# Kernel optimization log

Hardware: AMD Instinct MI355X
Metric: run time of the kernel (lower is better)

Reference implementation:

```python
import jax, jax.numpy as jnp
import numpy as np

C = 256

def setup_inputs() -> dict:
    key = jax.random.key(0)
    ks = jax.random.split(key, 7)
    s = 1.0 / np.sqrt(C)
    x = jax.random.normal(ks[0], (4, C, 64, 64), dtype=jnp.float32)
    Wq = jax.random.uniform(ks[1], (C, C), jnp.float32, -s, s)
    bq = jax.random.uniform(ks[2], (C,), jnp.float32, -s, s)
    Wk = jax.random.uniform(ks[3], (C, C), jnp.float32, -s, s)
    bk = jax.random.uniform(ks[4], (C,), jnp.float32, -s, s)
    Wv = jax.random.uniform(ks[5], (C, C), jnp.float32, -s, s)
    bv = jax.random.uniform(ks[6], (C,), jnp.float32, -s, s)
    return {"x": x, "Wq": Wq, "bq": bq, "Wk": Wk, "bk": bk, "Wv": Wv, "bv": bv}

def reference(x, Wq, bq, Wk, bk, Wv, bv):
    B, Cc, H, W = x.shape
    N = H * W
    xf = x.reshape(B, Cc, N)                      # (B, C, N)
    # 1x1 conv == channel linear: out[b,o,n] = sum_c W[o,c] x[b,c,n] + b[o]
    q = jnp.einsum('oc,bcn->bno', Wq, xf) + bq    # (B, N, C)  proj_query^T
    k = jnp.einsum('oc,bcn->bon', Wk, xf) + bk[None, :, None]  # (B, C, N)
    v = jnp.einsum('oc,bcn->bon', Wv, xf) + bv[None, :, None]  # (B, C, N)
    energy = jnp.einsum('bnc,bcm->bnm', q, k)     # (B, N, N)
    attention = jax.nn.softmax(energy, axis=-1)
    # out = V @ attention^T : out[b,c,n] = sum_m v[b,c,m] * attention[b,n,m]
    out = jnp.einsum('bcm,bnm->bcn', v, attention)
    return out.reshape(B, Cc, H, W)
```

## Files before the change

kernel.cpp:

```cpp
#include <hip/hip_runtime.h>
#include <math.h>

#define BB 4
#define CC 256
#define NN 4096

using half8 = __attribute__((ext_vector_type(8))) _Float16;
using f32x4 = __attribute__((ext_vector_type(4))) float;

__device__ __forceinline__ unsigned short f2h(float f) {
  _Float16 h = (_Float16)f;
  return __builtin_bit_cast(unsigned short, h);
}

#define ASYNC16(g, l)                                                        \
  __builtin_amdgcn_global_load_lds(                                          \
      (const __attribute__((address_space(1))) unsigned int*)(g),            \
      (__attribute__((address_space(3))) unsigned int*)(l), 16, 0, 0)

__device__ __forceinline__ int kt_off(int r, int chunk) {
  return r * 256 + (((chunk & 24) | ((chunk ^ r) & 7)) << 3);
}
__device__ __forceinline__ int vt_off(int r, int chunk) {
  return r * 64 + (((chunk ^ r) & 7) << 3);
}

__global__ __launch_bounds__(256) void k_transpose(const float* __restrict__ x,
                                                   unsigned short* __restrict__ Xt) {
  __shared__ float tile[64][65];
  int b = blockIdx.z, c0 = blockIdx.y * 64, n0 = blockIdx.x * 64;
  int t = threadIdx.x;
  const float* xp = x + ((size_t)b * CC + c0) * NN + n0;
#pragma unroll
  for (int p = 0; p < 4; ++p) {
    int c = p * 16 + (t >> 4);
    int j = (t & 15) * 4;
    float4 v = *(const float4*)(xp + (size_t)c * NN + j);
    tile[c][j] = v.x; tile[c][j + 1] = v.y; tile[c][j + 2] = v.z; tile[c][j + 3] = v.w;
  }
  __syncthreads();
  unsigned short* xtp = Xt + ((size_t)b * NN + n0) * CC + c0;
#pragma unroll
  for (int p = 0; p < 2; ++p) {
    int n = p * 32 + (t >> 3);
    int cb = (t & 7) * 8;
    union { unsigned short u[8]; uint4 v; } tmp;
#pragma unroll
    for (int i = 0; i < 8; ++i) tmp.u[i] = f2h(tile[cb + i][n]);
    *(uint4*)(xtp + (size_t)n * CC + cb) = tmp.v;
  }
}

__global__ __launch_bounds__(256, 1) void k_proj(const unsigned short* __restrict__ Xt,
    const float* __restrict__ Wq, const float* __restrict__ bq,
    const float* __restrict__ Wk, const float* __restrict__ bk,
    const float* __restrict__ Wv, const float* __restrict__ bv,
    unsigned short* __restrict__ Q, unsigned short* __restrict__ K,
    unsigned short* __restrict__ V) {
  __shared__ union {
    struct { unsigned short xa[128][72]; unsigned short wb[256][72]; } s;
    unsigned short qo[128][264];
    unsigned short vo[256][136];
  } u;
  int proj = blockIdx.z;
  const float* W    = proj == 0 ? Wq : (proj == 1 ? Wk : Wv);
  const float* bias = proj == 0 ? bq : (proj == 1 ? bk : bv);
  int b = blockIdx.y, n0 = blockIdx.x * 128;
  int t = threadIdx.x, w = t >> 6, lane = t & 63, l15 = lane & 15, quad = lane >> 4;

  f32x4 z = {0.f, 0.f, 0.f, 0.f};
  f32x4 acc[2][16];
#pragma unroll
  for (int i = 0; i < 2; ++i)
#pragma unroll
    for (int j = 0; j < 16; ++j) acc[i][j] = z;

  for (int ks = 0; ks < 4; ++ks) {
    __syncthreads();
#pragma unroll
    for (int p = 0; p < 4; ++p) {
      int r = p * 32 + (t >> 3);
      *(uint4*)&u.s.xa[r][(t & 7) * 8] =
        *(const uint4*)(Xt + ((size_t)b * NN + n0 + r) * CC + ks * 64 + (t & 7) * 8);
    }
#pragma unroll
    for (int p = 0; p < 16; ++p) {
      int r = p * 16 + (t >> 4);
      float4 wv = *(const float4*)(W + (size_t)r * CC + ks * 64 + (t & 15) * 4);
      ushort4 pk;
      pk.x = f2h(wv.x); pk.y = f2h(wv.y); pk.z = f2h(wv.z); pk.w = f2h(wv.w);
      *(ushort4*)&u.s.wb[r][(t & 15) * 4] = pk;
    }
    __syncthreads();
#pragma unroll
    for (int kc = 0; kc < 2; ++kc) {
      half8 af[2];
#pragma unroll
      for (int nt = 0; nt < 2; ++nt)
        af[nt] = *(const half8*)&u.s.xa[w * 32 + nt * 16 + l15][kc * 32 + quad * 8];
#pragma unroll
      for (int ct = 0; ct < 16; ++ct) {
        half8 bf = *(const half8*)&u.s.wb[ct * 16 + l15][kc * 32 + quad * 8];
        acc[0][ct] = __builtin_amdgcn_mfma_f32_16x16x32_f16(af[0], bf, acc[0][ct], 0, 0, 0);
        acc[1][ct] = __builtin_amdgcn_mfma_f32_16x16x32_f16(af[1], bf, acc[1][ct], 0, 0, 0);
      }
    }
  }
#pragma unroll
  for (int ct = 0; ct < 16; ++ct) {
    float bv_ = bias[ct * 16 + l15];
#pragma unroll
    for (int nt = 0; nt < 2; ++nt)
#pragma unroll
      for (int r = 0; r < 4; ++r) acc[nt][ct][r] += bv_;
  }
  __syncthreads();
  if (proj < 2) {
#pragma unroll
    for (int nt = 0; nt < 2; ++nt)
#pragma unroll
      for (int ct = 0; ct < 16; ++ct)
#pragma unroll
        for (int r = 0; r < 4; ++r)
          u.qo[w * 32 + nt * 16 + quad * 4 + r][ct * 16 + l15] = f2h(acc[nt][ct][r]);
    __syncthreads();
    unsigned short* out = (proj == 0 ? Q : K) + ((size_t)b * NN + n0) * CC;
#pragma unroll
    for (int p = 0; p < 16; ++p) {
      int f = p * 4096 + t * 16;
      int n = f >> 9, ob = f & 511;
      *(uint4*)((char*)out + (size_t)n * 512 + ob) =
        *(const uint4*)((const char*)&u.qo[n][0] + ob);
    }
  } else {
#pragma unroll
    for (int nt = 0; nt < 2; ++nt)
#pragma unroll
      for (int ct = 0; ct < 16; ++ct)
#pragma unroll
        for (int r = 0; r < 4; ++r)
          u.vo[ct * 16 + l15][w * 32 + nt * 16 + quad * 4 + r] = f2h(acc[nt][ct][r]);
    __syncthreads();
    unsigned short* out = V + (size_t)b * CC * NN + n0;
#pragma unroll
    for (int p = 0; p < 16; ++p) {
      int o = p * 16 + (t >> 4);
      *(uint4*)((char*)out + (size_t)o * NN * 2 + (t & 15) * 16) =
        *(const uint4*)&u.vo[o][(t & 15) * 8];
    }
  }
}

__global__ __launch_bounds__(512) void k_flash(const unsigned short* __restrict__ Q,
    const unsigned short* __restrict__ K, const unsigned short* __restrict__ V,
    float* __restrict__ out, float* __restrict__ opart, float* __restrict__ ml,
    int n_splits) {
  __shared__ unsigned short ktA[16384], ktB[16384];
  __shared__ unsigned short vtA[16384], vtB[16384];
  __shared__ unsigned short pt[8192];
  int b = blockIdx.y, q0 = blockIdx.x * 128, split = blockIdx.z;
  int nper = 64 / n_splits;
  int t = threadIdx.x, w = t >> 6, lane = t & 63, l15 = lane & 15, quad = lane >> 4;

  half8 qf[8];
  const unsigned short* qrow = Q + ((size_t)b * NN + q0 + w * 16 + l15) * CC;
#pragma unroll
  for (int k = 0; k < 8; ++k) qf[k] = *(const half8*)(qrow + k * 32 + quad * 8);

  f32x4 z = {0.f, 0.f, 0.f, 0.f};
  f32x4 o_acc[16];
#pragma unroll
  for (int i = 0; i < 16; ++i) o_acc[i] = z;
  float m_i[4], lp_[4];
#pragma unroll
  for (int r = 0; r < 4; ++r) { m_i[r] = -INFINITY; lp_[r] = 0.f; }

  int it_beg = split * nper, it_end = it_beg + nper;

  auto dma_k = [&](int it, unsigned short* dst) {
    const char* kb = (const char*)(K + ((size_t)b * NN + it * 64) * CC);
#pragma unroll
    for (int p = 0; p < 4; ++p) {
      int c = p * 512 + t;
      int r = c >> 5, lo = c & 31;
      int chunk = (lo & 24) | ((lo ^ r) & 7);
      ASYNC16(kb + r * 512 + chunk * 16, &dst[(p * 512 + (w << 6)) * 8]);
    }
  };
  auto dma_v = [&](int it, unsigned short* dst) {
    const char* vb = (const char*)(V + (size_t)b * CC * NN + it * 64);
#pragma unroll
    for (int p = 0; p < 4; ++p) {
      int c = p * 512 + t;
      int r = c >> 3;
      int chunk = (c ^ r) & 7;
      ASYNC16(vb + (size_t)r * 8192 + chunk * 16, &dst[(p * 512 + (w << 6)) * 8]);
    }
  };

  auto body = [&](const unsigned short* ktc, const unsigned short* vtc,
                  unsigned short* ktn, unsigned short* vtn, int it) {
    if (it + 1 < it_end) { dma_k(it + 1, ktn); dma_v(it + 1, vtn); }

    f32x4 sa[4];
#pragma unroll
    for (int j = 0; j < 4; ++j) sa[j] = z;
#pragma unroll
    for (int k = 0; k < 8; ++k) {
#pragma unroll
      for (int j = 0; j < 4; ++j) {
        half8 bf = *(const half8*)&ktc[kt_off(j * 16 + l15, 4 * k + quad)];
        sa[j] = __builtin_amdgcn_mfma_f32_16x16x32_f16(qf[k], bf, sa[j], 0, 0, 0);
      }
    }
    float mt[4];
#pragma unroll
    for (int r = 0; r < 4; ++r)
      mt[r] = fmaxf(fmaxf(sa[0][r], sa[1][r]), fmaxf(sa[2][r], sa[3][r]));
#pragma unroll
    for (int off = 1; off < 16; off <<= 1)
#pragma unroll
      for (int r = 0; r < 4; ++r)
        mt[r] = fmaxf(mt[r], __shfl_xor(mt[r], off, 64));
    float alpha[4];
#pragma unroll
    for (int r = 0; r < 4; ++r) {
      float mn = fmaxf(m_i[r], mt[r]);
      alpha[r] = __expf(m_i[r] - mn);
      m_i[r] = mn;
    }
#pragma unroll
    for (int r = 0; r < 4; ++r) {
      float ls = 0.f;
#pragma unroll
      for (int j = 0; j < 4; ++j) {
        float p = __expf(sa[j][r] - m_i[r]);
        sa[j][r] = p;
        ls += p;
      }
      lp_[r] = lp_[r] * alpha[r] + ls;
    }
#pragma unroll
    for (int ct = 0; ct < 16; ++ct)
#pragma unroll
      for (int r = 0; r < 4; ++r) o_acc[ct][r] *= alpha[r];
#pragma unroll
    for (int j = 0; j < 4; ++j)
#pragma unroll
      for (int r = 0; r < 4; ++r) {
        int row = quad * 4 + r;
        int chunk = 2 * j + (l15 >> 3);
        pt[w * 1024 + row * 64 + (((chunk ^ row) & 7) << 3) + (l15 & 7)] = f2h(sa[j][r]);
      }
#pragma unroll
    for (int mc = 0; mc < 2; ++mc) {
      half8 af = *(const half8*)&pt[w * 1024 + l15 * 64 + ((((mc * 4 + quad) ^ l15) & 7) << 3)];
#pragma unroll
      for (int ct = 0; ct < 16; ++ct) {
        half8 bf = *(const half8*)&vtc[vt_off(ct * 16 + l15, mc * 4 + quad)];
        o_acc[ct] = __builtin_amdgcn_mfma_f32_16x16x32_f16(af, bf, o_acc[ct], 0, 0, 0);
      }
    }
    __syncthreads();
  };

  dma_k(it_beg, ktA);
  dma_v(it_beg, vtA);
  __syncthreads();

  for (int it = it_beg; it < it_end; it += 2) {
    body(ktA, vtA, ktB, vtB, it);
    body(ktB, vtB, ktA, vtA, it + 1);
  }

#pragma unroll
  for (int off = 1; off < 16; off <<= 1)
#pragma unroll
    for (int r = 0; r < 4; ++r)
      lp_[r] += __shfl_xor(lp_[r], off, 64);

  float sc[4];
#pragma unroll
  for (int r = 0; r < 4; ++r) sc[r] = (n_splits == 1) ? 1.f / lp_[r] : 1.f;

  float (*od)[128] = (float(*)[128])ktA;
  float* ob = (n_splits == 1 ? out : opart + (size_t)split * BB * CC * NN)
              + (size_t)b * CC * NN + q0;
#pragma unroll
  for (int qtr = 0; qtr < 4; ++qtr) {
    __syncthreads();
#pragma unroll
    for (int ct2 = 0; ct2 < 4; ++ct2) {
      int ct = qtr * 4 + ct2;
#pragma unroll
      for (int r = 0; r < 4; ++r)
        od[ct2 * 16 + l15][w * 16 + quad * 4 + r] = o_acc[ct][r] * sc[r];
    }
    __syncthreads();
#pragma unroll
    for (int pp = 0; pp < 4; ++pp) {
      int row = pp * 16 + (t >> 5);
      *(float4*)(ob + (size_t)(qtr * 64 + row) * NN + (t & 31) * 4) =
        *(const float4*)&od[row][(t & 31) * 4];
    }
  }
  if (n_splits != 1 && l15 == 0) {
    float* mp = ml + ((size_t)(split * 2 + 0) * BB + b) * NN + q0 + w * 16 + quad * 4;
    float* lq = ml + ((size_t)(split * 2 + 1) * BB + b) * NN + q0 + w * 16 + quad * 4;
#pragma unroll
    for (int r = 0; r < 4; ++r) { mp[r] = m_i[r]; lq[r] = lp_[r]; }
  }
}

__global__ __launch_bounds__(256) void k_merge(const float* __restrict__ opart,
    const float* __restrict__ ml, float* __restrict__ out) {
  size_t i = ((size_t)blockIdx.x * 256 + threadIdx.x) * 4;
  int n = (int)(i & (NN - 1));
  int b = (int)(i >> 20);
  float4 m1 = *(const float4*)(ml + (size_t)(0 * BB + b) * NN + n);
  float4 l1 = *(const float4*)(ml + (size_t)(1 * BB + b) * NN + n);
  float4 m2 = *(const float4*)(ml + (size_t)(2 * BB + b) * NN + n);
  float4 l2 = *(const float4*)(ml + (size_t)(3 * BB + b) * NN + n);
  float4 o1 = *(const float4*)(opart + i);
  float4 o2 = *(const float4*)(opart + (size_t)BB * CC * NN + i);
  float4 o;
#define MERGE1(f) { \
    float mm = fmaxf(m1.f, m2.f); \
    float e1 = __expf(m1.f - mm), e2 = __expf(m2.f - mm); \
    o.f = (e1 * o1.f + e2 * o2.f) / (e1 * l1.f + e2 * l2.f); }
  MERGE1(x) MERGE1(y) MERGE1(z) MERGE1(w)
#undef MERGE1
  *(float4*)(out + i) = o;
}

extern "C" void kernel_launch(void* const* d_in, const int* in_sizes, int n_in,
                              void* d_out, int out_size, void* d_ws, size_t ws_size,
                              hipStream_t stream) {
  const float* x  = (const float*)d_in[0];
  const float* Wq = (const float*)d_in[1];
  const float* bq = (const float*)d_in[2];
  const float* Wk = (const float*)d_in[3];
  const float* bk = (const float*)d_in[4];
  const float* Wv = (const float*)d_in[5];
  const float* bv = (const float*)d_in[6];
  float* out = (float*)d_out;
  char* ws = (char*)d_ws;
  unsigned short* Xt = (unsigned short*)(ws);
  unsigned short* Qb = (unsigned short*)(ws + (size_t)8  * 1024 * 1024);
  unsigned short* Kb = (unsigned short*)(ws + (size_t)16 * 1024 * 1024);
  unsigned short* Vb = (unsigned short*)(ws + (size_t)24 * 1024 * 1024);
  float* Opart = (float*)(ws + (size_t)32 * 1024 * 1024);
  float* Ml    = (float*)(ws + (size_t)64 * 1024 * 1024);

  k_transpose<<<dim3(64, 4, 4), 256, 0, stream>>>(x, Xt);
  k_proj<<<dim3(32, 4, 3), 256, 0, stream>>>(Xt, Wq, bq, Wk, bk, Wv, bv, Qb, Kb, Vb);

  bool split2 = ws_size >= (size_t)68 * 1024 * 1024;
  if (split2) {
    k_flash<<<dim3(32, 4, 2), 512, 0, stream>>>(Qb, Kb, Vb, out, Opart, Ml, 2);
    k_merge<<<dim3(4096), 256, 0, stream>>>(Opart, Ml, out);
  } else {
    k_flash<<<dim3(32, 4, 1), 512, 0, stream>>>(Qb, Kb, Vb, out, Opart, Ml, 1);
  }
}
```

Before: 219.3 us.

## Split flash attention 4-way with fp16 partials, single-buffered smem, pre-cast weights

Adds a kernel that casts the weights to fp16 once. The projection kernel now stages the whole weight matrix in LDS through async loads and runs with 512 threads. The flash kernel drops K/V double-buffering in favor of a smaller shared-memory footprint. It splits the key range 4 ways instead of 2 for more blocks per GPU, storing partial outputs in fp16 to cut merge traffic. The costs are added precision loss in the partials, an extra launch, and less load/compute overlap inside flash.

```diff
diff --git a/kernel.cpp b/kernel.cpp
--- a/kernel.cpp
+++ b/kernel.cpp
@@ -11,6 +11,9 @@
 __device__ __forceinline__ unsigned short f2h(float f) {
   _Float16 h = (_Float16)f;
   return __builtin_bit_cast(unsigned short, h);
+}
+__device__ __forceinline__ float h2f(unsigned short u) {
+  return (float)__builtin_bit_cast(_Float16, u);
 }
 
 #define ASYNC16(g, l)                                                        \
@@ -18,7 +21,7 @@
       (const __attribute__((address_space(1))) unsigned int*)(g),            \
       (__attribute__((address_space(3))) unsigned int*)(l), 16, 0, 0)
 
-__device__ __forceinline__ int kt_off(int r, int chunk) {
+__device__ __forceinline__ int row512_off(int r, int chunk) {
   return r * 256 + (((chunk & 24) | ((chunk ^ r) & 7)) << 3);
 }
 __device__ __forceinline__ int vt_off(int r, int chunk) {
@@ -51,58 +54,62 @@
   }
 }
 
-__global__ __launch_bounds__(256, 1) void k_proj(const unsigned short* __restrict__ Xt,
-    const float* __restrict__ Wq, const float* __restrict__ bq,
-    const float* __restrict__ Wk, const float* __restrict__ bk,
-    const float* __restrict__ Wv, const float* __restrict__ bv,
+__global__ __launch_bounds__(256) void k_wcast(const float* __restrict__ Wq,
+    const float* __restrict__ Wk, const float* __restrict__ Wv,
+    unsigned short* __restrict__ Wh) {
+  const float* W = blockIdx.y == 0 ? Wq : (blockIdx.y == 1 ? Wk : Wv);
+  int idx = blockIdx.x * 1024 + threadIdx.x * 4;
+  float4 v = *(const float4*)(W + idx);
+  union { unsigned short u[4]; uint2 v2; } pk;
+  pk.u[0] = f2h(v.x); pk.u[1] = f2h(v.y); pk.u[2] = f2h(v.z); pk.u[3] = f2h(v.w);
+  *(uint2*)(Wh + blockIdx.y * 65536 + idx) = pk.v2;
+}
+
+__global__ __launch_bounds__(512) void k_proj(const unsigned short* __restrict__ Xt,
+    const unsigned short* __restrict__ Wh,
+    const float* __restrict__ bq, const float* __restrict__ bk,
+    const float* __restrict__ bv,
     unsigned short* __restrict__ Q, unsigned short* __restrict__ K,
     unsigned short* __restrict__ V) {
-  __shared__ union {
-    struct { unsigned short xa[128][72]; unsigned short wb[256][72]; } s;
-    unsigned short qo[128][264];
-    unsigned short vo[256][136];
-  } u;
-  int proj = blockIdx.z;
-  const float* W    = proj == 0 ? Wq : (proj == 1 ? Wk : Wv);
+  __shared__ unsigned short ps[73728];
+  unsigned short* wh = ps;
+  unsigned short* xa = ps + 65536;
+  int proj = blockIdx.z, b = blockIdx.y, n0 = blockIdx.x * 128;
+  int t = threadIdx.x, w = t >> 6, lane = t & 63, l15 = lane & 15, quad = lane >> 4;
+  const unsigned short* Wp = Wh + proj * 65536;
   const float* bias = proj == 0 ? bq : (proj == 1 ? bk : bv);
-  int b = blockIdx.y, n0 = blockIdx.x * 128;
-  int t = threadIdx.x, w = t >> 6, lane = t & 63, l15 = lane & 15, quad = lane >> 4;
+
+#pragma unroll
+  for (int p = 0; p < 16; ++p) {
+    int c = p * 512 + t;
+    int r = c >> 5, lo = c & 31;
+    int ch = (lo & 24) | ((lo ^ r) & 7);
+    ASYNC16((const char*)Wp + r * 512 + ch * 16, &wh[(p * 512 + (w << 6)) * 8]);
+  }
 
   f32x4 z = {0.f, 0.f, 0.f, 0.f};
-  f32x4 acc[2][16];
-#pragma unroll
-  for (int i = 0; i < 2; ++i)
-#pragma unroll
-    for (int j = 0; j < 16; ++j) acc[i][j] = z;
+  f32x4 acc[16];
+#pragma unroll
+  for (int i = 0; i < 16; ++i) acc[i] = z;
 
   for (int ks = 0; ks < 4; ++ks) {
-    __syncthreads();
-#pragma unroll
-    for (int p = 0; p < 4; ++p) {
-      int r = p * 32 + (t >> 3);
-      *(uint4*)&u.s.xa[r][(t & 7) * 8] =
-        *(const uint4*)(Xt + ((size_t)b * NN + n0 + r) * CC + ks * 64 + (t & 7) * 8);
-    }
-#pragma unroll
-    for (int p = 0; p < 16; ++p) {
-      int r = p * 16 + (t >> 4);
-      float4 wv = *(const float4*)(W + (size_t)r * CC + ks * 64 + (t & 15) * 4);
-      ushort4 pk;
-      pk.x = f2h(wv.x); pk.y = f2h(wv.y); pk.z = f2h(wv.z); pk.w = f2h(wv.w);
-      *(ushort4*)&u.s.wb[r][(t & 15) * 4] = pk;
+    if (ks) __syncthreads();
+#pragma unroll
+    for (int p = 0; p < 2; ++p) {
+      int c = p * 512 + t;
+      int r = c >> 3;
+      int ch = (c ^ r) & 7;
+      ASYNC16((const char*)(Xt + ((size_t)b * NN + n0 + r) * CC + ks * 64) + ch * 16,
+              &xa[(p * 512 + (w << 6)) * 8]);
     }
     __syncthreads();
 #pragma unroll
     for (int kc = 0; kc < 2; ++kc) {
-      half8 af[2];
-#pragma unroll
-      for (int nt = 0; nt < 2; ++nt)
-        af[nt] = *(const half8*)&u.s.xa[w * 32 + nt * 16 + l15][kc * 32 + quad * 8];
+      half8 af = *(const half8*)&xa[vt_off(w * 16 + l15, kc * 4 + quad)];
 #pragma unroll
       for (int ct = 0; ct < 16; ++ct) {
-        half8 bf = *(const half8*)&u.s.wb[ct * 16 + l15][kc * 32 + quad * 8];
-        acc[0][ct] = __builtin_amdgcn_mfma_f32_16x16x32_f16(af[0], bf, acc[0][ct], 0, 0, 0);
-        acc[1][ct] = __builtin_amdgcn_mfma_f32_16x16x32_f16(af[1], bf, acc[1][ct], 0, 0, 0);
+        half8 bf = *(const half8*)&wh[row512_off(ct * 16 + l15, ks * 8 + kc * 4 + quad)];
+        acc[ct] = __builtin_amdgcn_mfma_f32_16x16x32_f16(af, bf, acc[ct], 0, 0, 0);
       }
     }
   }
@@ -110,54 +117,51 @@
   for (int ct = 0; ct < 16; ++ct) {
     float bv_ = bias[ct * 16 + l15];
 #pragma unroll
-    for (int nt = 0; nt < 2; ++nt)
-#pragma unroll
-      for (int r = 0; r < 4; ++r) acc[nt][ct][r] += bv_;
+    for (int r = 0; r < 4; ++r) acc[ct][r] += bv_;
   }
   __syncthreads();
   if (proj < 2) {
-#pragma unroll
-    for (int nt = 0; nt < 2; ++nt)
-#pragma unroll
-      for (int ct = 0; ct < 16; ++ct)
-#pragma unroll
-        for (int r = 0; r < 4; ++r)
-          u.qo[w * 32 + nt * 16 + quad * 4 + r][ct * 16 + l15] = f2h(acc[nt][ct][r]);
-    __syncthreads();
-    unsigned short* out = (proj == 0 ? Q : K) + ((size_t)b * NN + n0) * CC;
-#pragma unroll
-    for (int p = 0; p < 16; ++p) {
-      int f = p * 4096 + t * 16;
-      int n = f >> 9, ob = f & 511;
-      *(uint4*)((char*)out + (size_t)n * 512 + ob) =
-        *(const uint4*)((const char*)&u.qo[n][0] + ob);
+    unsigned short (*qo)[264] = (unsigned short(*)[264])ps;
+#pragma unroll
+    for (int ct = 0; ct < 16; ++ct)
+#pragma unroll
+      for (int r = 0; r < 4; ++r)
+        qo[w * 16 + quad * 4 + r][ct * 16 + l15] = f2h(acc[ct][r]);
+    __syncthreads();
+    unsigned short* outp = (proj == 0 ? Q : K) + ((size_t)b * NN + n0) * CC;
+#pragma unroll
+    for (int p = 0; p < 8; ++p) {
+      int f = p * 8192 + t * 16;
+      int n = f >> 9, off = f & 511;
+      *(uint4*)((char*)outp + (size_t)n * 512 + off) =
+        *(const uint4*)((const char*)&qo[n][0] + off);
     }
   } else {
-#pragma unroll
-    for (int nt = 0; nt < 2; ++nt)
-#pragma unroll
-      for (int ct = 0; ct < 16; ++ct)
-#pragma unroll
-        for (int r = 0; r < 4; ++r)
-          u.vo[ct * 16 + l15][w * 32 + nt * 16 + quad * 4 + r] = f2h(acc[nt][ct][r]);
-    __syncthreads();
-    unsigned short* out = V + (size_t)b * CC * NN + n0;
-#pragma unroll
-    for (int p = 0; p < 16; ++p) {
-      int o = p * 16 + (t >> 4);
-      *(uint4*)((char*)out + (size_t)o * NN * 2 + (t & 15) * 16) =
-        *(const uint4*)&u.vo[o][(t & 15) * 8];
+    unsigned short (*vo)[132] = (unsigned short(*)[132])ps;
+#pragma unroll
+    for (int ct = 0; ct < 16; ++ct)
+#pragma unroll
+      for (int r = 0; r < 4; ++r)
+        vo[ct * 16 + l15][w * 16 + quad * 4 + r] = f2h(acc[ct][r]);
+    __syncthreads();
+#pragma unroll
+    for (int p = 0; p < 8; ++p) {
+      int f = p * 8192 + t * 16;
+      int o = f >> 8, off = f & 255;
+      *(uint4*)((char*)V + (((size_t)b * CC + o) * NN + n0) * 2 + off) =
+        *(const uint4*)((const char*)&vo[o][0] + off);
     }
   }
 }
 
 __global__ __launch_bounds__(512) void k_flash(const unsigned short* __restrict__ Q,
     const unsigned short* __restrict__ K, const unsigned short* __restrict__ V,
-    float* __restrict__ out, float* __restrict__ opart, float* __restrict__ ml,
-    int n_splits) {
-  __shared__ unsigned short ktA[16384], ktB[16384];
-  __shared__ unsigned short vtA[16384], vtB[16384];
-  __shared__ unsigned short pt[8192];
+    float* __restrict__ out, unsigned short* __restrict__ opart,
+    float* __restrict__ ml, int n_splits) {
+  __shared__ unsigned short smem[36864];
+  unsigned short* kt = smem;
+  unsigned short* vt = smem + 16384;
+  unsigned short* pt = smem + 32768;
   int b = blockIdx.y, q0 = blockIdx.x * 128, split = blockIdx.z;
   int nper = 64 / n_splits;
   int t = threadIdx.x, w = t >> 6, lane = t & 63, l15 = lane & 15, quad = lane >> 4;
@@ -177,42 +181,47 @@
 
   int it_beg = split * nper, it_end = it_beg + nper;
 
-  auto dma_k = [&](int it, unsigned short* dst) {
+  auto dma_k = [&](int it) {
     const char* kb = (const char*)(K + ((size_t)b * NN + it * 64) * CC);
 #pragma unroll
     for (int p = 0; p < 4; ++p) {
       int c = p * 512 + t;
       int r = c >> 5, lo = c & 31;
-      int chunk = (lo & 24) | ((lo ^ r) & 7);
-      ASYNC16(kb + r * 512 + chunk * 16, &dst[(p * 512 + (w << 6)) * 8]);
+      int ch = (lo & 24) | ((lo ^ r) & 7);
+      ASYNC16(kb + r * 512 + ch * 16, &kt[(p * 512 + (w << 6)) * 8]);
     }
   };
-  auto dma_v = [&](int it, unsigned short* dst) {
+  auto dma_v = [&](int it) {
     const char* vb = (const char*)(V + (size_t)b * CC * NN + it * 64);
 #pragma unroll
     for (int p = 0; p < 4; ++p) {
       int c = p * 512 + t;
       int r = c >> 3;
-      int chunk = (c ^ r) & 7;
-      ASYNC16(vb + (size_t)r * 8192 + chunk * 16, &dst[(p * 512 + (w << 6)) * 8]);
+      int ch = (c ^ r) & 7;
+      ASYNC16(vb + (size_t)r * 8192 + ch * 16, &vt[(p * 512 + (w << 6)) * 8]);
     }
   };
 
-  auto body = [&](const unsigned short* ktc, const unsigned short* vtc,
-                  unsigned short* ktn, unsigned short* vtn, int it) {
-    if (it + 1 < it_end) { dma_k(it + 1, ktn); dma_v(it + 1, vtn); }
+  dma_k(it_beg);
+  __syncthreads();
+
+  for (int it = it_beg; it < it_end; ++it) {
+    dma_v(it);
 
     f32x4 sa[4];
 #pragma unroll
     for (int j = 0; j < 4; ++j) sa[j] = z;
 #pragma unroll
-    for (int k = 0; k < 8; ++k) {
+    for (int kk = 0; kk < 8; ++kk) {
 #pragma unroll
       for (int j = 0; j < 4; ++j) {
-        half8 bf = *(const half8*)&ktc[kt_off(j * 16 + l15, 4 * k + quad)];
-        sa[j] = __builtin_amdgcn_mfma_f32_16x16x32_f16(qf[k], bf, sa[j], 0, 0, 0);
-      }
-    }
+        half8 bf = *(const half8*)&kt[row512_off(j * 16 + l15, kk * 4 + quad)];
+        sa[j] = __builtin_amdgcn_mfma_f32_16x16x32_f16(qf[kk], bf, sa[j], 0, 0, 0);
+      }
+    }
+    __syncthreads();
+    if (it + 1 < it_end) dma_k(it + 1);
+
     float mt[4];
 #pragma unroll
     for (int r = 0; r < 4; ++r)
@@ -244,33 +253,27 @@
     for (int ct = 0; ct < 16; ++ct)
 #pragma unroll
       for (int r = 0; r < 4; ++r) o_acc[ct][r] *= alpha[r];
-#pragma unroll
-    for (int j = 0; j < 4; ++j)
-#pragma unroll
-      for (int r = 0; r < 4; ++r) {
-        int row = quad * 4 + r;
-        int chunk = 2 * j + (l15 >> 3);
-        pt[w * 1024 + row * 64 + (((chunk ^ row) & 7) << 3) + (l15 & 7)] = f2h(sa[j][r]);
-      }
-#pragma unroll
-    for (int mc = 0; mc < 2; ++mc) {
-      half8 af = *(const half8*)&pt[w * 1024 + l15 * 64 + ((((mc * 4 + quad) ^ l15) & 7) << 3)];
+
+#pragma unroll
+    for (int hf = 0; hf < 2; ++hf) {
+#pragma unroll
+      for (int j2 = 0; j2 < 2; ++j2) {
+#pragma unroll
+        for (int r = 0; r < 4; ++r) {
+          int row = quad * 4 + r;
+          int ch = 2 * j2 + (l15 >> 3);
+          pt[w * 512 + row * 32 + (((ch ^ row) & 3) << 3) + (l15 & 7)] =
+              f2h(sa[hf * 2 + j2][r]);
+        }
+      }
+      half8 af = *(const half8*)&pt[w * 512 + l15 * 32 + (((quad ^ l15) & 3) << 3)];
 #pragma unroll
       for (int ct = 0; ct < 16; ++ct) {
-        half8 bf = *(const half8*)&vtc[vt_off(ct * 16 + l15, mc * 4 + quad)];
+        half8 bf = *(const half8*)&vt[vt_off(ct * 16 + l15, hf * 4 + quad)];
         o_acc[ct] = __builtin_amdgcn_mfma_f32_16x16x32_f16(af, bf, o_acc[ct], 0, 0, 0);
       }
     }
     __syncthreads();
-  };
-
-  dma_k(it_beg, ktA);
-  dma_v(it_beg, vtA);
-  __syncthreads();
-
-  for (int it = it_beg; it < it_end; it += 2) {
-    body(ktA, vtA, ktB, vtB, it);
-    body(ktB, vtB, ktA, vtA, it + 1);
   }
 
 #pragma unroll
@@ -283,54 +286,73 @@
 #pragma unroll
   for (int r = 0; r < 4; ++r) sc[r] = (n_splits == 1) ? 1.f / lp_[r] : 1.f;
 
-  float (*od)[128] = (float(*)[128])ktA;
-  float* ob = (n_splits == 1 ? out : opart + (size_t)split * BB * CC * NN)
-              + (size_t)b * CC * NN + q0;
+  float* od = (float*)smem;
+  float* obf = out + (size_t)b * CC * NN + q0;
+  unsigned short* obh = opart + ((size_t)split * BB + b) * CC * NN + q0;
 #pragma unroll
   for (int qtr = 0; qtr < 4; ++qtr) {
     __syncthreads();
 #pragma unroll
-    for (int ct2 = 0; ct2 < 4; ++ct2) {
-      int ct = qtr * 4 + ct2;
+    for (int cp = 0; cp < 4; ++cp) {
+      int ct = qtr * 4 + cp;
 #pragma unroll
       for (int r = 0; r < 4; ++r)
-        od[ct2 * 16 + l15][w * 16 + quad * 4 + r] = o_acc[ct][r] * sc[r];
-    }
-    __syncthreads();
-#pragma unroll
-    for (int pp = 0; pp < 4; ++pp) {
-      int row = pp * 16 + (t >> 5);
-      *(float4*)(ob + (size_t)(qtr * 64 + row) * NN + (t & 31) * 4) =
-        *(const float4*)&od[row][(t & 31) * 4];
+        od[(cp * 16 + l15) * 132 + w * 16 + quad * 4 + r] = o_acc[ct][r] * sc[r];
+    }
+    __syncthreads();
+    if (n_splits == 1) {
+#pragma unroll
+      for (int p2 = 0; p2 < 4; ++p2) {
+        int row = p2 * 16 + (t >> 5);
+        *(float4*)(obf + (size_t)(qtr * 64 + row) * NN + (t & 31) * 4) =
+          *(const float4*)&od[row * 132 + (t & 31) * 4];
+      }
+    } else {
+#pragma unroll
+      for (int p2 = 0; p2 < 2; ++p2) {
+        int row = p2 * 32 + (t >> 4);
+        int q8 = (t & 15) * 8;
+        union { unsigned short u[8]; uint4 v4; } tmp;
+#pragma unroll
+        for (int i2 = 0; i2 < 8; ++i2) tmp.u[i2] = f2h(od[row * 132 + q8 + i2]);
+        *(uint4*)(obh + (size_t)(qtr * 64 + row) * NN + q8) = tmp.v4;
+      }
     }
   }
   if (n_splits != 1 && l15 == 0) {
-    float* mp = ml + ((size_t)(split * 2 + 0) * BB + b) * NN + q0 + w * 16 + quad * 4;
-    float* lq = ml + ((size_t)(split * 2 + 1) * BB + b) * NN + q0 + w * 16 + quad * 4;
+    size_t qi = (size_t)q0 + w * 16 + quad * 4;
+    float* mp = ml + ((size_t)(split * 2 + 0) * BB + b) * NN + qi;
+    float* lq = ml + ((size_t)(split * 2 + 1) * BB + b) * NN + qi;
 #pragma unroll
     for (int r = 0; r < 4; ++r) { mp[r] = m_i[r]; lq[r] = lp_[r]; }
   }
 }
 
-__global__ __launch_bounds__(256) void k_merge(const float* __restrict__ opart,
+__global__ __launch_bounds__(256) void k_merge(const unsigned short* __restrict__ opart,
     const float* __restrict__ ml, float* __restrict__ out) {
   size_t i = ((size_t)blockIdx.x * 256 + threadIdx.x) * 4;
   int n = (int)(i & (NN - 1));
   int b = (int)(i >> 20);
-  float4 m1 = *(const float4*)(ml + (size_t)(0 * BB + b) * NN + n);
-  float4 l1 = *(const float4*)(ml + (size_t)(1 * BB + b) * NN + n);
-  float4 m2 = *(const float4*)(ml + (size_t)(2 * BB + b) * NN + n);
-  float4 l2 = *(const float4*)(ml + (size_t)(3 * BB + b) * NN + n);
-  float4 o1 = *(const float4*)(opart + i);
-  float4 o2 = *(const float4*)(opart + (size_t)BB * CC * NN + i);
-  float4 o;
-#define MERGE1(f) { \
-    float mm = fmaxf(m1.f, m2.f); \
-    float e1 = __expf(m1.f - mm), e2 = __expf(m2.f - mm); \
-    o.f = (e1 * o1.f + e2 * o2.f) / (e1 * l1.f + e2 * l2.f); }
-  MERGE1(x) MERGE1(y) MERGE1(z) MERGE1(w)
-#undef MERGE1
-  *(float4*)(out + i) = o;
+  float4 m[4], l[4];
+  ushort4 o[4];
+#pragma unroll
+  for (int s = 0; s < 4; ++s) {
+    m[s] = *(const float4*)(ml + ((size_t)(s * 2 + 0) * BB + b) * NN + n);
+    l[s] = *(const float4*)(ml + ((size_t)(s * 2 + 1) * BB + b) * NN + n);
+    o[s] = *(const ushort4*)(opart + (size_t)s * BB * CC * NN + i);
+  }
+  float4 res;
+#define MRG(f, comp) { \
+    float M = fmaxf(fmaxf(m[0].f, m[1].f), fmaxf(m[2].f, m[3].f)); \
+    float num = 0.f, den = 0.f; \
+    num += __expf(m[0].f - M) * h2f(o[0].comp); den += __expf(m[0].f - M) * l[0].f; \
+    num += __expf(m[1].f - M) * h2f(o[1].comp); den += __expf(m[1].f - M) * l[1].f; \
+    num += __expf(m[2].f - M) * h2f(o[2].comp); den += __expf(m[2].f - M) * l[2].f; \
+    num += __expf(m[3].f - M) * h2f(o[3].comp); den += __expf(m[3].f - M) * l[3].f; \
+    res.f = num / den; }
+  MRG(x, x) MRG(y, y) MRG(z, z) MRG(w, w)
+#undef MRG
+  *(float4*)(out + i) = res;
 }
 
 extern "C" void kernel_launch(void* const* d_in, const int* in_sizes, int n_in,
@@ -345,21 +367,20 @@
   const float* bv = (const float*)d_in[6];
   float* out = (float*)d_out;
   char* ws = (char*)d_ws;
-  unsigned short* Xt = (unsigned short*)(ws);
-  unsigned short* Qb = (unsigned short*)(ws + (size_t)8  * 1024 * 1024);
-  unsigned short* Kb = (unsigned short*)(ws + (size_t)16 * 1024 * 1024);
-  unsigned short* Vb = (unsigned short*)(ws + (size_t)24 * 1024 * 1024);
-  float* Opart = (float*)(ws + (size_t)32 * 1024 * 1024);
-  float* Ml    = (float*)(ws + (size_t)64 * 1024 * 1024);
-
+  const size_t MB = 1024 * 1024;
+  unsigned short* Qb = (unsigned short*)(ws);
+  unsigned short* Kb = (unsigned short*)(ws + 8 * MB);
+  unsigned short* Vb = (unsigned short*)(ws + 16 * MB);
+  unsigned short* Xt = (unsigned short*)(ws + 24 * MB);
+  unsigned short* Wh = (unsigned short*)(ws + 32 * MB);
+  float*          Ml = (float*)(ws + 33 * MB);
+  unsigned short* Op = (unsigned short*)(ws + 34 * MB);
+
+  k_wcast<<<dim3(64, 3), 256, 0, stream>>>(Wq, Wk, Wv, Wh);
   k_transpose<<<dim3(64, 4, 4), 256, 0, stream>>>(x, Xt);
-  k_proj<<<dim3(32, 4, 3), 256, 0, stream>>>(Xt, Wq, bq, Wk, bk, Wv, bv, Qb, Kb, Vb);
-
-  bool split2 = ws_size >= (size_t)68 * 1024 * 1024;
-  if (split2) {
-    k_flash<<<dim3(32, 4, 2), 512, 0, stream>>>(Qb, Kb, Vb, out, Opart, Ml, 2);
-    k_merge<<<dim3(4096), 256, 0, stream>>>(Opart, Ml, out);
-  } else {
-    k_flash<<<dim3(32, 4, 1), 512, 0, stream>>>(Qb, Kb, Vb, out, Opart, Ml, 1);
-  }
-}
+  k_proj<<<dim3(32, 4, 3), 512, 0, stream>>>(Xt, Wh, bq, bk, bv, Qb, Kb, Vb);
+
+  int ns = (ws_size >= 66 * MB) ? 4 : 1;
+  k_flash<<<dim3(32, 4, ns), 512, 0, stream>>>(Qb, Kb, Vb, out, Op, Ml, ns);
+  if (ns == 4) k_merge<<<dim3(4096), 256, 0, stream>>>(Op, Ml, out);
+}
```

Result: slower. 230.6 us (+5.2%).
